# Performance work log

Measured on AMD Instinct MI355X. Metric: run time of the kernel, lower is better.

Reference implementation:

```python
import jax, jax.numpy as jnp
import numpy as np
import math

B, S, HID, H = 8, 512, 768, 12
D = HID // H  # 64
LABEL_VOCAB = 2 * 40 + 1  # 81
EPS = 1e-5


def layernorm(x, g, b):
    mu = jnp.mean(x, axis=-1, keepdims=True)
    var = jnp.var(x, axis=-1, keepdims=True)
    return (x - mu) * jax.lax.rsqrt(var + EPS) * g + b


def setup_inputs() -> dict:
    key = jax.random.key(0)
    ks = jax.random.split(key, 12)
    s = 0.02
    return {
        "hidden_states": jax.random.normal(ks[0], (B, S, HID), jnp.float32),
        "attention_mask": jnp.zeros((B, 1, 1, S), jnp.float32),
        "graph_arc": jax.random.randint(ks[1], (B, S, S), 0, LABEL_VOCAB, jnp.int32),
        "Wq": jax.random.normal(ks[2], (HID, HID), jnp.float32) * s,
        "bq": jnp.zeros((HID,), jnp.float32),
        "Wk": jax.random.normal(ks[3], (HID, HID), jnp.float32) * s,
        "bk": jnp.zeros((HID,), jnp.float32),
        "Wv": jax.random.normal(ks[4], (HID, HID), jnp.float32) * s,
        "bv": jnp.zeros((HID,), jnp.float32),
        "rel_k": jax.random.normal(ks[5], (LABEL_VOCAB, D), jnp.float32) * s,
        "rel_v": jax.random.normal(ks[6], (LABEL_VOCAB, D), jnp.float32) * s,
        "ln_k_g": jnp.ones((D,), jnp.float32),
        "ln_k_b": jnp.zeros((D,), jnp.float32),
        "ln_v_g": jnp.ones((D,), jnp.float32),
        "ln_v_b": jnp.zeros((D,), jnp.float32),
    }


def reference(hidden_states, attention_mask, graph_arc, Wq, bq, Wk, bk, Wv, bv,
              rel_k, rel_v, ln_k_g, ln_k_b, ln_v_g, ln_v_b):
    # projections -> [B, H, S, D]
    def split_heads(x):
        return x.reshape(B, S, H, D).transpose(0, 2, 1, 3)

    q = split_heads(hidden_states @ Wq + bq)
    k = split_heads(hidden_states @ Wk + bk)
    v = split_heads(hidden_states @ Wv + bv)

    # relation embeddings [B, S, S, D], layernormed over D
    dp_keys = layernorm(rel_k[graph_arc], ln_k_g, ln_k_b)
    dp_values = layernorm(rel_v[graph_arc], ln_v_g, ln_v_b)

    scores = jnp.einsum('bhqd,bhkd->bhqk', q, k) / math.sqrt(D)
    # relative_matmul_dp: per (b, q-position) GEMM of q[B,S,H,D] with dp_keys^T
    scores = scores + jnp.einsum('bqhd,bqkd->bhqk', q.transpose(0, 2, 1, 3), dp_keys)
    scores = scores + attention_mask

    probs = jax.nn.softmax(scores, axis=-1)  # dropout p=0 (eval)

    ctx = jnp.einsum('bhqk,bhkd->bqhd', probs, v)
    # relative_matmul_dpv
    ctx = ctx + jnp.einsum('bhqk,bqkd->bqhd', probs, dp_values)
    return ctx.reshape(B, S, HID)
```

## Files before the change

kernel.cpp:

```cpp
#include <hip/hip_runtime.h>
#include <hip/hip_bf16.h>

#define BB 8
#define SS 512
#define HIDV 768
#define HH 12
#define DD 64
#define LV 81

typedef __attribute__((ext_vector_type(8))) short short8v;
typedef __attribute__((ext_vector_type(4))) short short4v;
typedef __attribute__((ext_vector_type(4))) float f32x4;

#define MFMA16(a, b, c) __builtin_amdgcn_mfma_f32_16x16x32_bf16(a, b, c, 0, 0, 0)

__device__ __forceinline__ short f2bf(float f) {
    __hip_bfloat16 h = __float2bfloat16(f);
    return *reinterpret_cast<short*>(&h);
}
__device__ __forceinline__ void gload16(const void* g, void* l) {
    __builtin_amdgcn_global_load_lds((const __attribute__((address_space(1))) void*)g,
                                     (__attribute__((address_space(3))) void*)l, 16, 0, 0);
}

__global__ __launch_bounds__(256) void prep_ln_kernel(
    const float* __restrict__ rel_k, const float* __restrict__ rel_v,
    const float* __restrict__ gk, const float* __restrict__ bk,
    const float* __restrict__ gv, const float* __restrict__ bv,
    short* __restrict__ lnkb, short* __restrict__ lnvT) {
    int t = threadIdx.x;
    if (t < 192) {
        bool isv = (t >= 96);
        int r = isv ? t - 96 : t;
        if (r < LV) {
            const float* row = (isv ? rel_v : rel_k) + r * DD;
            const float* g = isv ? gv : gk;
            const float* be = isv ? bv : bk;
            float mu = 0.f;
            for (int d = 0; d < DD; ++d) mu += row[d];
            mu *= (1.f / DD);
            float var = 0.f;
            for (int d = 0; d < DD; ++d) { float x = row[d] - mu; var += x * x; }
            var *= (1.f / DD);
            float rs = rsqrtf(var + 1e-5f);
            if (!isv) {
                for (int d = 0; d < DD; ++d)
                    lnkb[r * DD + d] = f2bf((row[d] - mu) * rs * g[d] + be[d]);
            } else {
                for (int d = 0; d < DD; ++d)
                    lnvT[d * 96 + r] = f2bf((row[d] - mu) * rs * g[d] + be[d]);
            }
        } else {
            if (!isv) for (int d = 0; d < DD; ++d) lnkb[r * DD + d] = 0;
            else      for (int d = 0; d < DD; ++d) lnvT[d * 96 + r] = 0;
        }
    }
}

#define NCONV 3072
#define NTRANS 1728
#define NARC 64
__global__ __launch_bounds__(256) void prep_fused_kernel(
    const float* __restrict__ hidden, short* __restrict__ hbf,
    const float* __restrict__ Wq, const float* __restrict__ Wk, const float* __restrict__ Wv,
    short* __restrict__ WqT, short* __restrict__ WkT, short* __restrict__ WvT,
    const int* __restrict__ arc, unsigned int* __restrict__ arcP) {
    __shared__ unsigned int sbuf[64 * 129];
    const int bid = blockIdx.x;
    const int tid = threadIdx.x;

    if (bid < NCONV) {
        int i = (bid * 256 + tid) * 4;
        float4 v = *reinterpret_cast<const float4*>(&hidden[i]);
        short4v o; o[0] = f2bf(v.x); o[1] = f2bf(v.y); o[2] = f2bf(v.z); o[3] = f2bf(v.w);
        *reinterpret_cast<short4v*>(&hbf[i]) = o;
    } else if (bid < NCONV + NTRANS) {
        int e = bid - NCONV;
        int z = e / 576, rem = e - z * 576;
        int by = rem / 24, bxx = rem - by * 24;
        const float* W; short* O;
        if (z == 0) { W = Wq; O = WqT; }
        else if (z == 1) { W = Wk; O = WkT; }
        else { W = Wv; O = WvT; }
        float* tile = reinterpret_cast<float*>(sbuf);
        int k0 = by * 32, n0 = bxx * 32;
        int r = tid >> 3, c4 = (tid & 7) * 4;
        float4 v = *reinterpret_cast<const float4*>(&W[(size_t)(k0 + r) * HIDV + n0 + c4]);
        tile[r * 33 + c4 + 0] = v.x; tile[r * 33 + c4 + 1] = v.y;
        tile[r * 33 + c4 + 2] = v.z; tile[r * 33 + c4 + 3] = v.w;
        __syncthreads();
        short4v o;
        o[0] = f2bf(tile[(c4 + 0) * 33 + r]); o[1] = f2bf(tile[(c4 + 1) * 33 + r]);
        o[2] = f2bf(tile[(c4 + 2) * 33 + r]); o[3] = f2bf(tile[(c4 + 3) * 33 + r]);
        *reinterpret_cast<short4v*>(&O[(size_t)(n0 + r) * HIDV + k0 + c4]) = o;
    } else {
        int e = bid - NCONV - NTRANS;
        int b = e >> 3, q0 = (e & 7) * 64;
        unsigned int* tbuf = sbuf;
        for (int i = tid; i < 64 * 128; i += 256) {
            int r = i >> 7, c4 = i & 127;
            int4 v = *reinterpret_cast<const int4*>(
                &arc[((size_t)(b * SS) + q0 + r) * SS + 4 * c4]);
            tbuf[r * 129 + c4] = (unsigned)(v.x & 255) | ((unsigned)(v.y & 255) << 8) |
                                 ((unsigned)(v.z & 255) << 16) | ((unsigned)(v.w & 255) << 24);
        }
        __syncthreads();
        for (int i = tid; i < 128 * 64; i += 256) {
            int k4 = i >> 6, r = i & 63;
            arcP[((size_t)b * 128 + k4) * SS + q0 + r] = tbuf[r * 129 + k4];
        }
    }
}

__global__ __launch_bounds__(256) void qkv_gemm_kernel(
    const short* __restrict__ Abf,
    const short* __restrict__ WqT, const short* __restrict__ WkT, const short* __restrict__ WvT,
    const float* __restrict__ bq, const float* __restrict__ bk, const float* __restrict__ bv,
    short* __restrict__ qo, short* __restrict__ ko, short* __restrict__ vto) {
    const short* Bt; const float* bias;
    int z = blockIdx.z;
    if (z == 0) { Bt = WqT; bias = bq; }
    else if (z == 1) { Bt = WkT; bias = bk; }
    else { Bt = WvT; bias = bv; }

    __shared__ short smem[8192];
    short* As = smem;
    short* Bs = smem + 4096;

    const int tid = threadIdx.x;
    const int lane = tid & 63, w = tid >> 6;
    const int li = lane & 15, g = lane >> 4;
    const int wr = w >> 1, wc = w & 1;
    const int m0 = blockIdx.y * 64, n0 = blockIdx.x * 64;

    f32x4 acc[2][2];
    for (int ra = 0; ra < 2; ++ra)
        for (int cb = 0; cb < 2; ++cb)
            for (int r = 0; r < 4; ++r) acc[ra][cb][r] = 0.f;

#pragma unroll 1
    for (int k0 = 0; k0 < HIDV; k0 += 64) {
#pragma unroll
        for (int j = 0; j < 2; ++j) {
            int c = j * 256 + tid;
            int row = c >> 3, s = c & 7;
            int src = s ^ (row & 7);
            gload16(Abf + (size_t)(m0 + row) * HIDV + k0 + src * 8, As + c * 8);
            gload16(Bt + (size_t)(n0 + row) * HIDV + k0 + src * 8, Bs + c * 8);
        }
        __syncthreads();
#pragma unroll
        for (int c = 0; c < 2; ++c) {
            short8v af[2], bf[2];
#pragma unroll
            for (int ra = 0; ra < 2; ++ra) {
                int row = 32 * wr + 16 * ra + li;
                int chunk = (4 * c + g) ^ (row & 7);
                af[ra] = *reinterpret_cast<const short8v*>(&As[row * 64 + chunk * 8]);
            }
#pragma unroll
            for (int cb = 0; cb < 2; ++cb) {
                int rowb = 32 * wc + 16 * cb + li;
                int chunk = (4 * c + g) ^ (rowb & 7);
                bf[cb] = *reinterpret_cast<const short8v*>(&Bs[rowb * 64 + chunk * 8]);
            }
#pragma unroll
            for (int ra = 0; ra < 2; ++ra)
#pragma unroll
                for (int cb = 0; cb < 2; ++cb)
                    acc[ra][cb] = MFMA16(af[ra], bf[cb], acc[ra][cb]);
        }
        __syncthreads();
    }

    const int h = n0 >> 6;
    const int bidx = m0 >> 9;
    if (z < 2) {
        short* dst = (z == 0) ? qo : ko;
        float sc = (z == 0) ? 1.f : 0.125f;
#pragma unroll
        for (int ra = 0; ra < 2; ++ra)
#pragma unroll
            for (int cb = 0; cb < 2; ++cb) {
                int n = 32 * wc + 16 * cb + li;
                float bv_ = bias[n0 + n];
#pragma unroll
                for (int r = 0; r < 4; ++r) {
                    int m = m0 + 32 * wr + 16 * ra + 4 * g + r;
                    int s = m & 511;
                    dst[(((size_t)bidx * HH + h) * SS + s) * DD + n] =
                        f2bf((acc[ra][cb][r] + bv_) * sc);
                }
            }
    } else {
        short* Cs = smem;
#pragma unroll
        for (int ra = 0; ra < 2; ++ra)
#pragma unroll
            for (int cb = 0; cb < 2; ++cb) {
                int nl = 32 * wc + 16 * cb + li;
                float bv_ = bias[n0 + nl];
#pragma unroll
                for (int r = 0; r < 4; ++r) {
                    int ml = 32 * wr + 16 * ra + 4 * g + r;
                    Cs[nl * 72 + ml] = f2bf(acc[ra][cb][r] + bv_);
                }
            }
        __syncthreads();
        for (int c = tid; c < 512; c += 256) {
            int dl = c >> 3, s8 = (c & 7) * 8;
            short8v vv = *reinterpret_cast<const short8v*>(&Cs[dl * 72 + s8]);
            *reinterpret_cast<short8v*>(
                &vto[(((size_t)bidx * HH + h) * DD + dl) * SS + (m0 & 511) + s8]) = vv;
        }
    }
}

__global__ __launch_bounds__(256, 2) void attn_kernel(
    const short* __restrict__ qb, const short* __restrict__ kb, const short* __restrict__ vt,
    const unsigned int* __restrict__ arcP, const float* __restrict__ maskp,
    const short* __restrict__ lnkb, const short* __restrict__ lnvT,
    float* __restrict__ outp) {
    __shared__ float qlds[4][16][84];
    __shared__ float bucket[4][16][100];

    const int tid = threadIdx.x;
    const int w = tid >> 6, lane = tid & 63;
    const int li = lane & 15, g = lane >> 4;
    const int bx = blockIdx.x;
    const int b = bx & 7;
    const int rest = bx >> 3;
    const int h = rest % HH, qt = rest / HH;
    const int bh = b * HH + h;
    const int q0 = qt * 64 + w * 16;

    const short* kbp = kb + (size_t)bh * SS * DD;
    const short* vbp = vt + (size_t)bh * DD * SS;
    const unsigned int* apb = arcP + (size_t)b * 128 * SS;
    const float* mkb = maskp + (size_t)b * SS;

    for (int i = lane; i < 16 * 100; i += 64) (&bucket[w][0][0])[i] = 0.f;

    short8v qf0, qf1;
    {
        const short* qrow = qb + ((size_t)bh * SS + q0 + li) * DD + 8 * g;
        qf0 = *reinterpret_cast<const short8v*>(qrow);
        qf1 = *reinterpret_cast<const short8v*>(qrow + 32);
    }

#pragma unroll
    for (int ct = 0; ct < 6; ++ct) {
        f32x4 a = {0.f, 0.f, 0.f, 0.f};
        short8v b0 = *reinterpret_cast<const short8v*>(&lnkb[(16 * ct + li) * DD + 8 * g]);
        short8v b1 = *reinterpret_cast<const short8v*>(&lnkb[(16 * ct + li) * DD + 32 + 8 * g]);
        a = MFMA16(qf0, b0, a);
        a = MFMA16(qf1, b1, a);
        if (16 * ct + li < 84)
#pragma unroll
            for (int r = 0; r < 4; ++r) qlds[w][4 * g + r][16 * ct + li] = a[r];
    }

    f32x4 oacc[4];
    for (int t = 0; t < 4; ++t) for (int r = 0; r < 4; ++r) oacc[t][r] = 0.f;

    short8v kf[8];
    short4v vreg[16];
    unsigned int a_[2][4];
    float4 m_[2][4];
    float qv_[2][16];
#pragma unroll
    for (int t = 0; t < 4; ++t) {
        const short* kr = kbp + (size_t)(16 * t + li) * DD + 8 * g;
        kf[2 * t] = *reinterpret_cast<const short8v*>(kr);
        kf[2 * t + 1] = *reinterpret_cast<const short8v*>(kr + 32);
        a_[0][t] = apb[(size_t)(4 * t + g) * SS + q0 + li];
        m_[0][t] = *reinterpret_cast<const float4*>(&mkb[16 * t + 4 * g]);
    }
#pragma unroll
    for (int t = 0; t < 4; ++t) {
        const unsigned int a4 = a_[0][t];
        qv_[0][4 * t + 0] = qlds[w][li][a4 & 255];
        qv_[0][4 * t + 1] = qlds[w][li][(a4 >> 8) & 255];
        qv_[0][4 * t + 2] = qlds[w][li][(a4 >> 16) & 255];
        qv_[0][4 * t + 3] = qlds[w][li][a4 >> 24];
    }

#pragma unroll
    for (int kt = 0; kt < 8; ++kt) {
        const int cur = kt & 1, nxt = cur ^ 1;
        const int kb0 = kt * 64;

        f32x4 sacc[4];
#pragma unroll
        for (int t = 0; t < 4; ++t) {
            f32x4 a = {0.f, 0.f, 0.f, 0.f};
            a = MFMA16(kf[2 * t], qf0, a);
            a = MFMA16(kf[2 * t + 1], qf1, a);
            sacc[t] = a;
        }

#pragma unroll
        for (int dt = 0; dt < 2; ++dt)
#pragma unroll
            for (int t2 = 0; t2 < 4; ++t2) {
                const short* vr = vbp + (size_t)(16 * t2 + li) * SS + kb0 + 32 * dt + 4 * g;
                vreg[8 * dt + 2 * t2 + 0] = *reinterpret_cast<const short4v*>(vr);
                vreg[8 * dt + 2 * t2 + 1] = *reinterpret_cast<const short4v*>(vr + 16);
            }
        if (kt < 7) {
#pragma unroll
            for (int t = 0; t < 4; ++t) {
                const short* kr = kbp + (size_t)(kb0 + 64 + 16 * t + li) * DD + 8 * g;
                kf[2 * t] = *reinterpret_cast<const short8v*>(kr);
                kf[2 * t + 1] = *reinterpret_cast<const short8v*>(kr + 32);
                a_[nxt][t] = apb[(size_t)((kt + 1) * 16 + 4 * t + g) * SS + q0 + li];
                m_[nxt][t] = *reinterpret_cast<const float4*>(&mkb[kb0 + 64 + 16 * t + 4 * g]);
            }
#pragma unroll
            for (int t = 0; t < 4; ++t) {
                const unsigned int a4 = a_[nxt][t];
                qv_[nxt][4 * t + 0] = qlds[w][li][a4 & 255];
                qv_[nxt][4 * t + 1] = qlds[w][li][(a4 >> 8) & 255];
                qv_[nxt][4 * t + 2] = qlds[w][li][(a4 >> 16) & 255];
                qv_[nxt][4 * t + 3] = qlds[w][li][a4 >> 24];
            }
        }

        float p[16];
#pragma unroll
        for (int t = 0; t < 4; ++t) {
            p[4 * t + 0] = __expf(sacc[t][0] + qv_[cur][4 * t + 0] + m_[cur][t].x);
            p[4 * t + 1] = __expf(sacc[t][1] + qv_[cur][4 * t + 1] + m_[cur][t].y);
            p[4 * t + 2] = __expf(sacc[t][2] + qv_[cur][4 * t + 2] + m_[cur][t].z);
            p[4 * t + 3] = __expf(sacc[t][3] + qv_[cur][4 * t + 3] + m_[cur][t].w);
        }

#pragma unroll
        for (int t = 0; t < 4; ++t) {
            const unsigned int a4 = a_[cur][t];
            unsafeAtomicAdd(&bucket[w][li][a4 & 255], p[4 * t + 0]);
            unsafeAtomicAdd(&bucket[w][li][(a4 >> 8) & 255], p[4 * t + 1]);
            unsafeAtomicAdd(&bucket[w][li][(a4 >> 16) & 255], p[4 * t + 2]);
            unsafeAtomicAdd(&bucket[w][li][a4 >> 24], p[4 * t + 3]);
        }

        short8v pfrag[2];
#pragma unroll
        for (int t = 0; t < 4; ++t)
#pragma unroll
            for (int r = 0; r < 4; ++r) pfrag[t >> 1][4 * (t & 1) + r] = f2bf(p[4 * t + r]);
#pragma unroll
        for (int dt = 0; dt < 2; ++dt) {
#pragma unroll
            for (int t2 = 0; t2 < 4; ++t2) {
                short4v v0 = vreg[8 * dt + 2 * t2 + 0];
                short4v v1 = vreg[8 * dt + 2 * t2 + 1];
                short8v vf;
                vf[0] = v0[0]; vf[1] = v0[1]; vf[2] = v0[2]; vf[3] = v0[3];
                vf[4] = v1[0]; vf[5] = v1[1]; vf[6] = v1[2]; vf[7] = v1[3];
                oacc[t2] = MFMA16(pfrag[dt], vf, oacc[t2]);
            }
        }
    }

    float lsum = 0.f;
#pragma unroll
    for (int j = 0; j < 24; ++j) {
        int c = 24 * g + j;
        lsum += (c < 81) ? bucket[w][li][c] : 0.f;
    }
    lsum += __shfl_xor(lsum, 16);
    lsum += __shfl_xor(lsum, 32);
    float inv = 1.f / lsum;
    float invr[4];
#pragma unroll
    for (int r = 0; r < 4; ++r) invr[r] = __shfl(inv, 4 * g + r);

    f32x4 racc[4];
    for (int t = 0; t < 4; ++t) for (int r = 0; r < 4; ++r) racc[t][r] = 0.f;
#pragma unroll
    for (int c = 0; c < 3; ++c) {
        f32x4 b0 = *reinterpret_cast<const f32x4*>(&bucket[w][li][8 * g + 32 * c]);
        f32x4 b1 = *reinterpret_cast<const f32x4*>(&bucket[w][li][8 * g + 32 * c + 4]);
        short8v bfr;
        bfr[0] = f2bf(b0[0]); bfr[1] = f2bf(b0[1]); bfr[2] = f2bf(b0[2]); bfr[3] = f2bf(b0[3]);
        bfr[4] = f2bf(b1[0]); bfr[5] = f2bf(b1[1]); bfr[6] = f2bf(b1[2]); bfr[7] = f2bf(b1[3]);
#pragma unroll
        for (int t2 = 0; t2 < 4; ++t2) {
            short8v lf = *reinterpret_cast<const short8v*>(
                &lnvT[(16 * t2 + li) * 96 + 8 * g + 32 * c]);
            racc[t2] = MFMA16(bfr, lf, racc[t2]);
        }
    }

#pragma unroll
    for (int t2 = 0; t2 < 4; ++t2)
#pragma unroll
        for (int r = 0; r < 4; ++r) {
            int row = q0 + 4 * g + r;
            outp[((size_t)b * SS + row) * HIDV + h * DD + 16 * t2 + li] =
                (oacc[t2][r] + racc[t2][r]) * invr[r];
        }
}

extern "C" void kernel_launch(void* const* d_in, const int* in_sizes, int n_in,
                              void* d_out, int out_size, void* d_ws, size_t ws_size,
                              hipStream_t stream) {
    const float* hidden = (const float*)d_in[0];
    const float* mask   = (const float*)d_in[1];
    const int*   arc    = (const int*)d_in[2];
    const float* Wq = (const float*)d_in[3];
    const float* bq = (const float*)d_in[4];
    const float* Wk = (const float*)d_in[5];
    const float* bk = (const float*)d_in[6];
    const float* Wv = (const float*)d_in[7];
    const float* bv = (const float*)d_in[8];
    const float* rel_k = (const float*)d_in[9];
    const float* rel_v = (const float*)d_in[10];
    const float* lng_k = (const float*)d_in[11];
    const float* lnb_k = (const float*)d_in[12];
    const float* lng_v = (const float*)d_in[13];
    const float* lnb_v = (const float*)d_in[14];
    float* out = (float*)d_out;

    char* p = (char*)d_ws;
    auto carve = [&](size_t bytes) { char* r = p; p += (bytes + 255) & ~(size_t)255; return r; };
    short* lnkb = (short*)carve((size_t)96 * DD * 2);
    short* lnvT = (short*)carve((size_t)DD * 96 * 2);
    short* hbf  = (short*)carve((size_t)BB * SS * HIDV * 2);
    short* WqT  = (short*)carve((size_t)HIDV * HIDV * 2);
    short* WkT  = (short*)carve((size_t)HIDV * HIDV * 2);
    short* WvT  = (short*)carve((size_t)HIDV * HIDV * 2);
    const size_t per = (size_t)BB * HH * SS * DD;
    short* qbuf = (short*)carve(per * 2);
    short* kbuf = (short*)carve(per * 2);
    short* vtb  = (short*)carve(per * 2);
    unsigned int* arcP = (unsigned int*)carve((size_t)BB * 128 * SS * 4);

    prep_ln_kernel<<<1, 256, 0, stream>>>(rel_k, rel_v, lng_k, lnb_k, lng_v, lnb_v, lnkb, lnvT);
    prep_fused_kernel<<<dim3(NCONV + NTRANS + NARC), 256, 0, stream>>>(
        hidden, hbf, Wq, Wk, Wv, WqT, WkT, WvT, arc, arcP);
    qkv_gemm_kernel<<<dim3(HIDV / 64, (BB * SS) / 64, 3), 256, 0, stream>>>(
        hbf, WqT, WkT, WvT, bq, bk, bv, qbuf, kbuf, vtb);
    attn_kernel<<<dim3(BB * HH * 8), 256, 0, stream>>>(
        qbuf, kbuf, vtb, arcP, mask, lnkb, lnvT, out);
}
```

Baseline: 192.1 us.

## Fold log2e into scores and use exp2, merged LDS table and packed bf16 conversion

Pre-scales the K projection, the relation-key table and the mask by log2(e) so the softmax can use the raw v_exp_f32 (exp2) instruction instead of __expf. The q-relation table and the probability bucket are merged into one LDS array, and the atomic add uses an inline ds_add_f32 with a fixed offset, so the same address register serves both the gather and the scatter. The prefetched gather of q·relk values is dropped and done inline, and bf16 conversions use the packed v_cvt_pk_bf16_f32 instruction. This trades some lost load prefetch overlap for fewer ALU ops and fewer address computations in the inner loop.

```diff
diff --git a/kernel.cpp b/kernel.cpp
--- a/kernel.cpp
+++ b/kernel.cpp
@@ -7,6 +7,7 @@
 #define HH 12
 #define DD 64
 #define LV 81
+#define LOG2E 1.44269504088896f
 
 typedef __attribute__((ext_vector_type(8))) short short8v;
 typedef __attribute__((ext_vector_type(4))) short short4v;
@@ -21,13 +22,27 @@
 __device__ __forceinline__ void gload16(const void* g, void* l) {
     __builtin_amdgcn_global_load_lds((const __attribute__((address_space(1))) void*)g,
                                      (__attribute__((address_space(3))) void*)l, 16, 0, 0);
+}
+__device__ __forceinline__ void ldsAddOff400(float* p, float v) {
+    __attribute__((address_space(3))) float* lp =
+        (__attribute__((address_space(3))) float*)p;
+    asm volatile("ds_add_f32 %0, %1 offset:400" : : "v"(lp), "v"(v) : "memory");
+}
+__device__ __forceinline__ float fexp2(float x) {
+    float r; asm("v_exp_f32 %0, %1" : "=v"(r) : "v"(x)); return r;
+}
+__device__ __forceinline__ unsigned cvtpk(float lo, float hi) {
+    unsigned r;
+    asm("v_cvt_pk_bf16_f32 %0, %1, %2" : "=v"(r) : "v"(lo), "v"(hi));
+    return r;
 }
 
 __global__ __launch_bounds__(256) void prep_ln_kernel(
     const float* __restrict__ rel_k, const float* __restrict__ rel_v,
     const float* __restrict__ gk, const float* __restrict__ bk,
     const float* __restrict__ gv, const float* __restrict__ bv,
-    short* __restrict__ lnkb, short* __restrict__ lnvT) {
+    const float* __restrict__ mask,
+    short* __restrict__ lnkb, short* __restrict__ lnvT, float* __restrict__ maskS) {
     int t = threadIdx.x;
     if (t < 192) {
         bool isv = (t >= 96);
@@ -45,7 +60,7 @@
             float rs = rsqrtf(var + 1e-5f);
             if (!isv) {
                 for (int d = 0; d < DD; ++d)
-                    lnkb[r * DD + d] = f2bf((row[d] - mu) * rs * g[d] + be[d]);
+                    lnkb[r * DD + d] = f2bf(((row[d] - mu) * rs * g[d] + be[d]) * LOG2E);
             } else {
                 for (int d = 0; d < DD; ++d)
                     lnvT[d * 96 + r] = f2bf((row[d] - mu) * rs * g[d] + be[d]);
@@ -54,6 +69,8 @@
             if (!isv) for (int d = 0; d < DD; ++d) lnkb[r * DD + d] = 0;
             else      for (int d = 0; d < DD; ++d) lnvT[d * 96 + r] = 0;
         }
+    } else {
+        for (int i = t - 192; i < BB * SS; i += 64) maskS[i] = mask[i] * LOG2E;
     }
 }
 
@@ -177,7 +194,7 @@
     const int bidx = m0 >> 9;
     if (z < 2) {
         short* dst = (z == 0) ? qo : ko;
-        float sc = (z == 0) ? 1.f : 0.125f;
+        float sc = (z == 0) ? 1.f : 0.125f * LOG2E;
 #pragma unroll
         for (int ra = 0; ra < 2; ++ra)
 #pragma unroll
@@ -218,11 +235,10 @@
 
 __global__ __launch_bounds__(256, 2) void attn_kernel(
     const short* __restrict__ qb, const short* __restrict__ kb, const short* __restrict__ vt,
-    const unsigned int* __restrict__ arcP, const float* __restrict__ maskp,
+    const unsigned int* __restrict__ arcP, const float* __restrict__ maskS,
     const short* __restrict__ lnkb, const short* __restrict__ lnvT,
     float* __restrict__ outp) {
-    __shared__ float qlds[4][16][84];
-    __shared__ float bucket[4][16][100];
+    __shared__ float tbl[4][16][200];
 
     const int tid = threadIdx.x;
     const int w = tid >> 6, lane = tid & 63;
@@ -237,9 +253,11 @@
     const short* kbp = kb + (size_t)bh * SS * DD;
     const short* vbp = vt + (size_t)bh * DD * SS;
     const unsigned int* apb = arcP + (size_t)b * 128 * SS;
-    const float* mkb = maskp + (size_t)b * SS;
-
-    for (int i = lane; i < 16 * 100; i += 64) (&bucket[w][0][0])[i] = 0.f;
+    const float* mkb = maskS + (size_t)b * SS;
+
+#pragma unroll
+    for (int rr = 0; rr < 16; ++rr)
+        for (int c = lane; c < 100; c += 64) tbl[w][rr][100 + c] = 0.f;
 
     short8v qf0, qf1;
     {
@@ -255,9 +273,8 @@
         short8v b1 = *reinterpret_cast<const short8v*>(&lnkb[(16 * ct + li) * DD + 32 + 8 * g]);
         a = MFMA16(qf0, b0, a);
         a = MFMA16(qf1, b1, a);
-        if (16 * ct + li < 84)
-#pragma unroll
-            for (int r = 0; r < 4; ++r) qlds[w][4 * g + r][16 * ct + li] = a[r];
+#pragma unroll
+        for (int r = 0; r < 4; ++r) tbl[w][4 * g + r][16 * ct + li] = a[r];
     }
 
     f32x4 oacc[4];
@@ -267,7 +284,6 @@
     short4v vreg[16];
     unsigned int a_[2][4];
     float4 m_[2][4];
-    float qv_[2][16];
 #pragma unroll
     for (int t = 0; t < 4; ++t) {
         const short* kr = kbp + (size_t)(16 * t + li) * DD + 8 * g;
@@ -276,14 +292,6 @@
         a_[0][t] = apb[(size_t)(4 * t + g) * SS + q0 + li];
         m_[0][t] = *reinterpret_cast<const float4*>(&mkb[16 * t + 4 * g]);
     }
-#pragma unroll
-    for (int t = 0; t < 4; ++t) {
-        const unsigned int a4 = a_[0][t];
-        qv_[0][4 * t + 0] = qlds[w][li][a4 & 255];
-        qv_[0][4 * t + 1] = qlds[w][li][(a4 >> 8) & 255];
-        qv_[0][4 * t + 2] = qlds[w][li][(a4 >> 16) & 255];
-        qv_[0][4 * t + 3] = qlds[w][li][a4 >> 24];
-    }
 
 #pragma unroll
     for (int kt = 0; kt < 8; ++kt) {
@@ -316,39 +324,33 @@
                 a_[nxt][t] = apb[(size_t)((kt + 1) * 16 + 4 * t + g) * SS + q0 + li];
                 m_[nxt][t] = *reinterpret_cast<const float4*>(&mkb[kb0 + 64 + 16 * t + 4 * g]);
             }
-#pragma unroll
-            for (int t = 0; t < 4; ++t) {
-                const unsigned int a4 = a_[nxt][t];
-                qv_[nxt][4 * t + 0] = qlds[w][li][a4 & 255];
-                qv_[nxt][4 * t + 1] = qlds[w][li][(a4 >> 8) & 255];
-                qv_[nxt][4 * t + 2] = qlds[w][li][(a4 >> 16) & 255];
-                qv_[nxt][4 * t + 3] = qlds[w][li][a4 >> 24];
-            }
         }
 
         float p[16];
-#pragma unroll
-        for (int t = 0; t < 4; ++t) {
-            p[4 * t + 0] = __expf(sacc[t][0] + qv_[cur][4 * t + 0] + m_[cur][t].x);
-            p[4 * t + 1] = __expf(sacc[t][1] + qv_[cur][4 * t + 1] + m_[cur][t].y);
-            p[4 * t + 2] = __expf(sacc[t][2] + qv_[cur][4 * t + 2] + m_[cur][t].z);
-            p[4 * t + 3] = __expf(sacc[t][3] + qv_[cur][4 * t + 3] + m_[cur][t].w);
-        }
-
 #pragma unroll
         for (int t = 0; t < 4; ++t) {
             const unsigned int a4 = a_[cur][t];
-            unsafeAtomicAdd(&bucket[w][li][a4 & 255], p[4 * t + 0]);
-            unsafeAtomicAdd(&bucket[w][li][(a4 >> 8) & 255], p[4 * t + 1]);
-            unsafeAtomicAdd(&bucket[w][li][(a4 >> 16) & 255], p[4 * t + 2]);
-            unsafeAtomicAdd(&bucket[w][li][a4 >> 24], p[4 * t + 3]);
-        }
-
+            float* g0 = &tbl[w][li][a4 & 255];
+            float* g1 = &tbl[w][li][(a4 >> 8) & 255];
+            float* g2 = &tbl[w][li][(a4 >> 16) & 255];
+            float* g3 = &tbl[w][li][a4 >> 24];
+            float p0 = fexp2(sacc[t][0] + *g0 + m_[cur][t].x);
+            float p1 = fexp2(sacc[t][1] + *g1 + m_[cur][t].y);
+            float p2 = fexp2(sacc[t][2] + *g2 + m_[cur][t].z);
+            float p3 = fexp2(sacc[t][3] + *g3 + m_[cur][t].w);
+            ldsAddOff400(g0, p0);
+            ldsAddOff400(g1, p1);
+            ldsAddOff400(g2, p2);
+            ldsAddOff400(g3, p3);
+            p[4 * t + 0] = p0; p[4 * t + 1] = p1; p[4 * t + 2] = p2; p[4 * t + 3] = p3;
+        }
+
+        unsigned pw[8];
+#pragma unroll
+        for (int i = 0; i < 8; ++i) pw[i] = cvtpk(p[2 * i], p[2 * i + 1]);
         short8v pfrag[2];
-#pragma unroll
-        for (int t = 0; t < 4; ++t)
-#pragma unroll
-            for (int r = 0; r < 4; ++r) pfrag[t >> 1][4 * (t & 1) + r] = f2bf(p[4 * t + r]);
+        pfrag[0] = *reinterpret_cast<short8v*>(&pw[0]);
+        pfrag[1] = *reinterpret_cast<short8v*>(&pw[4]);
 #pragma unroll
         for (int dt = 0; dt < 2; ++dt) {
 #pragma unroll
@@ -367,7 +369,7 @@
 #pragma unroll
     for (int j = 0; j < 24; ++j) {
         int c = 24 * g + j;
-        lsum += (c < 81) ? bucket[w][li][c] : 0.f;
+        lsum += (c < 81) ? tbl[w][li][100 + c] : 0.f;
     }
     lsum += __shfl_xor(lsum, 16);
     lsum += __shfl_xor(lsum, 32);
@@ -380,11 +382,12 @@
     for (int t = 0; t < 4; ++t) for (int r = 0; r < 4; ++r) racc[t][r] = 0.f;
 #pragma unroll
     for (int c = 0; c < 3; ++c) {
-        f32x4 b0 = *reinterpret_cast<const f32x4*>(&bucket[w][li][8 * g + 32 * c]);
-        f32x4 b1 = *reinterpret_cast<const f32x4*>(&bucket[w][li][8 * g + 32 * c + 4]);
-        short8v bfr;
-        bfr[0] = f2bf(b0[0]); bfr[1] = f2bf(b0[1]); bfr[2] = f2bf(b0[2]); bfr[3] = f2bf(b0[3]);
-        bfr[4] = f2bf(b1[0]); bfr[5] = f2bf(b1[1]); bfr[6] = f2bf(b1[2]); bfr[7] = f2bf(b1[3]);
+        f32x4 b0 = *reinterpret_cast<const f32x4*>(&tbl[w][li][100 + 8 * g + 32 * c]);
+        f32x4 b1 = *reinterpret_cast<const f32x4*>(&tbl[w][li][100 + 8 * g + 32 * c + 4]);
+        unsigned bw[4];
+        bw[0] = cvtpk(b0[0], b0[1]); bw[1] = cvtpk(b0[2], b0[3]);
+        bw[2] = cvtpk(b1[0], b1[1]); bw[3] = cvtpk(b1[2], b1[3]);
+        short8v bfr = *reinterpret_cast<short8v*>(&bw[0]);
 #pragma unroll
         for (int t2 = 0; t2 < 4; ++t2) {
             short8v lf = *reinterpret_cast<const short8v*>(
@@ -427,6 +430,7 @@
     auto carve = [&](size_t bytes) { char* r = p; p += (bytes + 255) & ~(size_t)255; return r; };
     short* lnkb = (short*)carve((size_t)96 * DD * 2);
     short* lnvT = (short*)carve((size_t)DD * 96 * 2);
+    float* maskS = (float*)carve((size_t)BB * SS * 4);
     short* hbf  = (short*)carve((size_t)BB * SS * HIDV * 2);
     short* WqT  = (short*)carve((size_t)HIDV * HIDV * 2);
     short* WkT  = (short*)carve((size_t)HIDV * HIDV * 2);
@@ -437,11 +441,12 @@
     short* vtb  = (short*)carve(per * 2);
     unsigned int* arcP = (unsigned int*)carve((size_t)BB * 128 * SS * 4);
 
-    prep_ln_kernel<<<1, 256, 0, stream>>>(rel_k, rel_v, lng_k, lnb_k, lng_v, lnb_v, lnkb, lnvT);
+    prep_ln_kernel<<<1, 256, 0, stream>>>(rel_k, rel_v, lng_k, lnb_k, lng_v, lnb_v,
+                                          mask, lnkb, lnvT, maskS);
     prep_fused_kernel<<<dim3(NCONV + NTRANS + NARC), 256, 0, stream>>>(
         hidden, hbf, Wq, Wk, Wv, WqT, WkT, WvT, arc, arcP);
     qkv_gemm_kernel<<<dim3(HIDV / 64, (BB * SS) / 64, 3), 256, 0, stream>>>(
         hbf, WqT, WkT, WvT, bq, bk, bv, qbuf, kbuf, vtb);
     attn_kernel<<<dim3(BB * HH * 8), 256, 0, stream>>>(
-        qbuf, kbuf, vtb, arcP, mask, lnkb, lnvT, out);
-}
+        qbuf, kbuf, vtb, arcP, maskS, lnkb, lnvT, out);
+}
```

Result: slower. 196.8 us (+2.5%).
